# Kernel optimization log

Measured on AMD Instinct MI355X. Metric: run time of the kernel, lower is better.

The kernel has to match this reference:

```python
import jax, jax.numpy as jnp
import numpy as np

B, IN, OUT = 2048, 64, 2048


def setup_inputs() -> dict:
    key = jax.random.key(0)
    k1, k2, k3 = jax.random.split(key, 3)
    x = jax.random.normal(k1, (B, IN), dtype=jnp.float32)
    # learned params (shapes per init: means [in, out], inv_std_dev [out, in, in])
    means = jax.random.uniform(k2, (IN, OUT), dtype=jnp.float32)
    # roughly like the inverse of a diagonal step matrix plus small noise
    inv_std_dev = (jax.random.normal(k3, (OUT, IN, IN), dtype=jnp.float32) * 0.05
                   + jnp.eye(IN, dtype=jnp.float32) * 0.5)
    return {"x": x, "means": means, "inv_std_dev": inv_std_dev}


def reference(x, means, inv_std_dev):
    # diff[b, o, i] = x[b, i] - means[i, o]   -> [B, OUT, IN]
    d = x[:, None, :] - means.T[None, :, :]
    # torch uses inv_std_dev.pow(2) (elementwise square), not a matrix square
    A = inv_std_dev * inv_std_dev  # [OUT, IN, IN]
    # per-neuron quadratic form: q[b, o] = d[b,o,:] @ A[o] @ d[b,o,:]
    q = jnp.einsum('boi,oij,boj->bo', d, A, d)
    return jnp.exp(-0.5 * q)  # [B, OUT]
```

## Files before the change

### kernel.cpp

```cpp
#include <hip/hip_runtime.h>
#include <hip/hip_bf16.h>

typedef __bf16 bf16x8 __attribute__((ext_vector_type(8)));
typedef float f32x4 __attribute__((ext_vector_type(4)));
typedef float f32x16 __attribute__((ext_vector_type(16)));

#define B_N 2048
#define O_N 2048
#define K_N 64

__device__ __forceinline__ void gld16(const void* g, void* l) {
    __builtin_amdgcn_global_load_lds(
        (const __attribute__((address_space(1))) void*)g,
        (__attribute__((address_space(3))) void*)l,
        16, 0, 0);
}

__global__ __launch_bounds__(256) void rbf_prep(
    const float* __restrict__ inv, const float* __restrict__ means,
    __bf16* __restrict__ Atp, __bf16* __restrict__ cPhi,
    __bf16* __restrict__ cPlo, float* __restrict__ kArr)
{
    __shared__ float s[64 * 65];
    __shared__ float mld[64];
    __shared__ float uw[128];
    const int o = blockIdx.x;
    const int t = threadIdx.x;
    const float4* src = (const float4*)(inv + (size_t)o * 4096);
#pragma unroll
    for (int k = 0; k < 4; ++k) {
        const int idx = k * 256 + t;
        const float4 v = src[idx];
        const int i = idx >> 4;
        const int j0 = (idx & 15) * 4;
        s[i * 65 + j0 + 0] = v.x * v.x;
        s[i * 65 + j0 + 1] = v.y * v.y;
        s[i * 65 + j0 + 2] = v.z * v.z;
        s[i * 65 + j0 + 3] = v.w * v.w;
    }
    if (t < 64) mld[t] = means[(size_t)t * O_N + o];
    __syncthreads();
    if (t < 64) {
        float u = 0.f;
#pragma unroll
        for (int i = 0; i < 64; ++i) u = fmaf(s[i * 65 + t], mld[i], u);
        uw[t] = u;
    } else if (t < 128) {
        const int j = t - 64;
        float w = 0.f;
#pragma unroll
        for (int i = 0; i < 64; ++i) w = fmaf(s[j * 65 + i], mld[i], w);
        uw[64 + j] = w;
    }
    __syncthreads();
    if (t < 64) {
        const float c = -(uw[t] + uw[64 + t]);
        const __bf16 hi = (__bf16)c;
        const __bf16 lo = (__bf16)(c - (float)hi);
        const size_t eidx = (size_t)(o >> 5) * 2048 + (size_t)(t >> 4) * 512
                          + (size_t)(o & 31) * 16 + (t & 15);
        cPhi[eidx] = hi;
        cPlo[eidx] = lo;
    }
    if (t == 0) {
        float kk = 0.f;
#pragma unroll
        for (int j = 0; j < 64; ++j) kk = fmaf(uw[j], mld[j], kk);
        kArr[o] = kk;
    }
#pragma unroll
    for (int r = 0; r < 2; ++r) {
        const int ch = r * 256 + t;
        const int ss = ch >> 7;
        const int j = (ch >> 1) & 63;
        const int h = ch & 1;
        bf16x8 v;
#pragma unroll
        for (int e = 0; e < 8; ++e)
            v[e] = (__bf16)s[(16 * ss + 8 * h + e) * 65 + j];
        *(bf16x8*)(Atp + (size_t)o * 4096 + (size_t)ch * 8) = v;
    }
}

__global__ __launch_bounds__(256, 4) void rbf_main(
    const float* __restrict__ x, const __bf16* __restrict__ Atp,
    const __bf16* __restrict__ cPhi, const __bf16* __restrict__ cPlo,
    const float* __restrict__ kArr, float* __restrict__ out)
{
    __shared__ __align__(16) __bf16 sA[2][4096];
    __shared__ __align__(16) float sLin[4][32][32];
    __shared__ float sK[32];

    const int tid = threadIdx.x;
    const int wave = tid >> 6;
    const int lane = tid & 63;
    const int b = lane & 31;
    const int h = lane >> 5;

    const int wg = (int)blockIdx.x;
    const int xcd = wg & 7;
    const int loc = wg >> 3;
    const int og = xcd * 8 + (loc >> 4);
    const int bg = loc & 15;
    const int oBase = og * 32;
    const int rowW = bg * 128 + wave * 32;
    const int row = rowW + b;
    const float* xr = x + (size_t)row * K_N;

    const f32x16 zz = {0.f,0.f,0.f,0.f,0.f,0.f,0.f,0.f,
                       0.f,0.f,0.f,0.f,0.f,0.f,0.f,0.f};

    bf16x8 xh[4], xl[4];
#pragma unroll
    for (int ss = 0; ss < 4; ++ss) {
        const float* p = xr + ss * 16 + h * 8;
        bf16x8 vh, vl;
#pragma unroll
        for (int e = 0; e < 8; ++e) {
            const float v = p[e];
            const __bf16 hi = (__bf16)v;
            vh[e] = hi;
            vl[e] = (__bf16)(v - (float)hi);
        }
        xh[ss] = vh; xl[ss] = vl;
    }
    f32x4 xd[2][4];
#pragma unroll
    for (int mt = 0; mt < 2; ++mt)
#pragma unroll
        for (int rq = 0; rq < 4; ++rq)
            xd[mt][rq] = *(const f32x4*)(xr + mt * 32 + rq * 8 + h * 4);

    {
        const __bf16* ch = cPhi + (size_t)og * 2048;
        const __bf16* cl = cPlo + (size_t)og * 2048;
        f32x16 lin = zz;
#pragma unroll
        for (int ss = 0; ss < 4; ++ss) {
            const bf16x8 fh = *(const bf16x8*)(ch + ss * 512 + b * 16 + h * 8);
            const bf16x8 fl = *(const bf16x8*)(cl + ss * 512 + b * 16 + h * 8);
            lin = __builtin_amdgcn_mfma_f32_32x32x16_bf16(fh, xh[ss], lin, 0, 0, 0);
            lin = __builtin_amdgcn_mfma_f32_32x32x16_bf16(fh, xl[ss], lin, 0, 0, 0);
            lin = __builtin_amdgcn_mfma_f32_32x32x16_bf16(fl, xh[ss], lin, 0, 0, 0);
        }
#pragma unroll
        for (int r = 0; r < 16; ++r)
            sLin[wave][(r & 3) + 8 * (r >> 2) + 4 * h][b] = lin[r];
    }
    if (tid < 32) sK[tid] = kArr[oBase + tid];

    const int L0 = tid * 16;
    const int L1 = 4096 + tid * 16;
    const int S0 = L0 ^ (((L0 >> 7) & 7) << 4);
    const int S1 = L1 ^ (((L1 >> 7) & 7) << 4);
    const char* gp = (const char*)(Atp + (size_t)oBase * 4096);
    gld16(gp + S0, (char*)&sA[0][0] + L0);
    gld16(gp + S1, (char*)&sA[0][0] + L1);

    const int off0 = (b * 32 + h * 16) ^ (((b >> 2) & 7) << 4);

    float q4[4];
#pragma unroll 4
    for (int i = 0; i < 32; ++i) {
        __syncthreads();
        if (i < 31) {
            const char* gn = gp + (size_t)(i + 1) * 8192;
            char* ld = (char*)&sA[(i + 1) & 1][0];
            gld16(gn + S0, ld + L0);
            gld16(gn + S1, ld + L1);
        }
        const char* bufp = (const char*)&sA[i & 1][0];

        f32x16 acc0 = zz, acc1 = zz;
#pragma unroll
        for (int ss = 0; ss < 4; ++ss) {
            const bf16x8 a0 = *(const bf16x8*)(bufp + ss * 2048 + off0);
            acc0 = __builtin_amdgcn_mfma_f32_32x32x16_bf16(a0, xh[ss], acc0, 0, 0, 0);
        }
#pragma unroll
        for (int ss = 0; ss < 4; ++ss) {
            const bf16x8 a1 = *(const bf16x8*)(bufp + ss * 2048 + 1024 + off0);
            acc1 = __builtin_amdgcn_mfma_f32_32x32x16_bf16(a1, xh[ss], acc1, 0, 0, 0);
        }

        float p[4] = {0.f, 0.f, 0.f, 0.f};
#pragma unroll
        for (int rg = 0; rg < 4; ++rg)
#pragma unroll
            for (int e = 0; e < 4; ++e)
                p[rg] = fmaf(acc0[rg * 4 + e], xd[0][rg][e], p[rg]);
#pragma unroll
        for (int rg = 0; rg < 4; ++rg)
#pragma unroll
            for (int e = 0; e < 4; ++e)
                p[rg] = fmaf(acc1[rg * 4 + e], xd[1][rg][e], p[rg]);
        float q = (p[0] + p[1]) + (p[2] + p[3]);
        q += __shfl_xor(q, 32, 64);
        q += sLin[wave][i][b];
        const float ev = exp2f((q + sK[i]) * -0.72134752044448170368f);
        q4[i & 3] = ev;

        if ((i & 3) == 3 && h == 0) {
            const f32x4 v = {q4[0], q4[1], q4[2], q4[3]};
            *(f32x4*)(out + (size_t)row * O_N + oBase + (i - 3)) = v;
        }
    }
}

extern "C" void kernel_launch(void* const* d_in, const int* in_sizes, int n_in,
                              void* d_out, int out_size, void* d_ws, size_t ws_size,
                              hipStream_t stream)
{
    const float* x = (const float*)d_in[0];
    const float* means = (const float*)d_in[1];
    const float* inv = (const float*)d_in[2];
    float* out = (float*)d_out;

    char* w = (char*)d_ws;
    __bf16* Atp  = (__bf16*)w;
    __bf16* cPhi = (__bf16*)(w + (size_t)O_N * 4096 * 2);
    __bf16* cPlo = (__bf16*)(w + (size_t)O_N * 4096 * 2 + 262144);
    float*  kArr = (float*)(w + (size_t)O_N * 4096 * 2 + 524288);

    rbf_prep<<<dim3(O_N), dim3(256), 0, stream>>>(inv, means, Atp, cPhi, cPlo, kArr);
    rbf_main<<<dim3(1024), dim3(256), 0, stream>>>(x, Atp, cPhi, cPlo, kArr, out);

    (void)in_sizes; (void)n_in; (void)out_size; (void)ws_size;
}
```

Before: 64.54 us.

## Double rows per wave, triple-buffer A tiles with explicit waitcnt pipeline

Each wave now handles 64 batch rows instead of 32, so every A tile loaded into LDS is reused across twice as many MFMAs, and the grid is halved to 512 workgroups. The LDS ring grows from double to triple buffering with a two-ahead prefetch, manual barriers and vmcnt waits, and s_setprio around the MFMA block. Outputs are now written as scalar stores per element instead of packed float4 stores. Launch bounds drop to 2 waves per SIMD to fit the extra registers, which lowers occupancy and may under-fill the 256 CUs with only 512 blocks.

```diff
diff --git a/kernel.cpp b/kernel.cpp
--- a/kernel.cpp
+++ b/kernel.cpp
@@ -73,22 +73,22 @@
         const int ch = r * 256 + t;
         const int ss = ch >> 7;
         const int j = (ch >> 1) & 63;
-        const int h = ch & 1;
+        const int hh = ch & 1;
         bf16x8 v;
 #pragma unroll
         for (int e = 0; e < 8; ++e)
-            v[e] = (__bf16)s[(16 * ss + 8 * h + e) * 65 + j];
+            v[e] = (__bf16)s[(16 * ss + 8 * hh + e) * 65 + j];
         *(bf16x8*)(Atp + (size_t)o * 4096 + (size_t)ch * 8) = v;
     }
 }
 
-__global__ __launch_bounds__(256, 4) void rbf_main(
+__global__ __launch_bounds__(256, 2) void rbf_main(
     const float* __restrict__ x, const __bf16* __restrict__ Atp,
     const __bf16* __restrict__ cPhi, const __bf16* __restrict__ cPlo,
     const float* __restrict__ kArr, float* __restrict__ out)
 {
-    __shared__ __align__(16) __bf16 sA[2][4096];
-    __shared__ __align__(16) float sLin[4][32][32];
+    __shared__ __align__(16) __bf16 sA[3][4096];
+    __shared__ __align__(16) float sLin[4][32][64];
     __shared__ float sK[32];
 
     const int tid = threadIdx.x;
@@ -100,111 +100,159 @@
     const int wg = (int)blockIdx.x;
     const int xcd = wg & 7;
     const int loc = wg >> 3;
-    const int og = xcd * 8 + (loc >> 4);
-    const int bg = loc & 15;
+    const int og = xcd * 8 + (loc >> 3);
+    const int bg = loc & 7;
     const int oBase = og * 32;
-    const int rowW = bg * 128 + wave * 32;
-    const int row = rowW + b;
-    const float* xr = x + (size_t)row * K_N;
+    const int rowW = bg * 256 + wave * 64;
+
+    const float* xr0 = x + (size_t)(rowW + b) * K_N;
+    const float* xr1 = x + (size_t)(rowW + 32 + b) * K_N;
 
     const f32x16 zz = {0.f,0.f,0.f,0.f,0.f,0.f,0.f,0.f,
                        0.f,0.f,0.f,0.f,0.f,0.f,0.f,0.f};
 
-    bf16x8 xh[4], xl[4];
-#pragma unroll
-    for (int ss = 0; ss < 4; ++ss) {
-        const float* p = xr + ss * 16 + h * 8;
-        bf16x8 vh, vl;
-#pragma unroll
-        for (int e = 0; e < 8; ++e) {
-            const float v = p[e];
-            const __bf16 hi = (__bf16)v;
-            vh[e] = hi;
-            vl[e] = (__bf16)(v - (float)hi);
-        }
-        xh[ss] = vh; xl[ss] = vl;
-    }
-    f32x4 xd[2][4];
-#pragma unroll
-    for (int mt = 0; mt < 2; ++mt)
-#pragma unroll
-        for (int rq = 0; rq < 4; ++rq)
-            xd[mt][rq] = *(const f32x4*)(xr + mt * 32 + rq * 8 + h * 4);
-
+    bf16x8 xh[2][4];
+    f32x4 xd[2][2][4];
     {
-        const __bf16* ch = cPhi + (size_t)og * 2048;
-        const __bf16* cl = cPlo + (size_t)og * 2048;
-        f32x16 lin = zz;
+        bf16x8 xl[2][4];
+#pragma unroll
+        for (int t = 0; t < 2; ++t) {
+            const float* xr = t ? xr1 : xr0;
+#pragma unroll
+            for (int ss = 0; ss < 4; ++ss) {
+                const float* p = xr + ss * 16 + h * 8;
+                bf16x8 vh, vl;
+#pragma unroll
+                for (int e = 0; e < 8; ++e) {
+                    const float v = p[e];
+                    const __bf16 hi = (__bf16)v;
+                    vh[e] = hi;
+                    vl[e] = (__bf16)(v - (float)hi);
+                }
+                xh[t][ss] = vh; xl[t][ss] = vl;
+            }
+#pragma unroll
+            for (int mt = 0; mt < 2; ++mt)
+#pragma unroll
+                for (int rq = 0; rq < 4; ++rq)
+                    xd[t][mt][rq] = *(const f32x4*)(xr + mt * 32 + rq * 8 + h * 4);
+        }
+        const __bf16* chp = cPhi + (size_t)og * 2048;
+        const __bf16* clp = cPlo + (size_t)og * 2048;
+        bf16x8 fh[4], fl[4];
 #pragma unroll
         for (int ss = 0; ss < 4; ++ss) {
-            const bf16x8 fh = *(const bf16x8*)(ch + ss * 512 + b * 16 + h * 8);
-            const bf16x8 fl = *(const bf16x8*)(cl + ss * 512 + b * 16 + h * 8);
-            lin = __builtin_amdgcn_mfma_f32_32x32x16_bf16(fh, xh[ss], lin, 0, 0, 0);
-            lin = __builtin_amdgcn_mfma_f32_32x32x16_bf16(fh, xl[ss], lin, 0, 0, 0);
-            lin = __builtin_amdgcn_mfma_f32_32x32x16_bf16(fl, xh[ss], lin, 0, 0, 0);
-        }
-#pragma unroll
-        for (int r = 0; r < 16; ++r)
-            sLin[wave][(r & 3) + 8 * (r >> 2) + 4 * h][b] = lin[r];
+            fh[ss] = *(const bf16x8*)(chp + ss * 512 + b * 16 + h * 8);
+            fl[ss] = *(const bf16x8*)(clp + ss * 512 + b * 16 + h * 8);
+        }
+#pragma unroll
+        for (int t = 0; t < 2; ++t) {
+            f32x16 lin = zz;
+#pragma unroll
+            for (int ss = 0; ss < 4; ++ss) {
+                lin = __builtin_amdgcn_mfma_f32_32x32x16_bf16(fh[ss], xh[t][ss], lin, 0, 0, 0);
+                lin = __builtin_amdgcn_mfma_f32_32x32x16_bf16(fh[ss], xl[t][ss], lin, 0, 0, 0);
+                lin = __builtin_amdgcn_mfma_f32_32x32x16_bf16(fl[ss], xh[t][ss], lin, 0, 0, 0);
+            }
+#pragma unroll
+            for (int r = 0; r < 16; ++r)
+                sLin[wave][(r & 3) + 8 * (r >> 2) + 4 * h][t * 32 + b] = lin[r];
+        }
     }
     if (tid < 32) sK[tid] = kArr[oBase + tid];
-
-    const int L0 = tid * 16;
-    const int L1 = 4096 + tid * 16;
+    __syncthreads();
+
+    const int L0 = tid * 16, L1 = 4096 + tid * 16;
     const int S0 = L0 ^ (((L0 >> 7) & 7) << 4);
     const int S1 = L1 ^ (((L1 >> 7) & 7) << 4);
     const char* gp = (const char*)(Atp + (size_t)oBase * 4096);
     gld16(gp + S0, (char*)&sA[0][0] + L0);
     gld16(gp + S1, (char*)&sA[0][0] + L1);
+    gld16(gp + 8192 + S0, (char*)&sA[1][0] + L0);
+    gld16(gp + 8192 + S1, (char*)&sA[1][0] + L1);
 
     const int off0 = (b * 32 + h * 16) ^ (((b >> 2) & 7) << 4);
-
-    float q4[4];
-#pragma unroll 4
-    for (int i = 0; i < 32; ++i) {
-        __syncthreads();
-        if (i < 31) {
-            const char* gn = gp + (size_t)(i + 1) * 8192;
-            char* ld = (char*)&sA[(i + 1) & 1][0];
-            gld16(gn + S0, ld + L0);
-            gld16(gn + S1, ld + L1);
-        }
-        const char* bufp = (const char*)&sA[i & 1][0];
-
-        f32x16 acc0 = zz, acc1 = zz;
+    float* o0 = out + (size_t)(rowW + b) * O_N + oBase;
+    float* o1 = out + (size_t)(rowW + 32 + b) * O_N + oBase;
+
+    auto body = [&](int i, const __bf16* bufp) {
+        __builtin_amdgcn_s_setprio(1);
+        f32x16 a00 = zz, a01 = zz, a10 = zz, a11 = zz;
 #pragma unroll
         for (int ss = 0; ss < 4; ++ss) {
-            const bf16x8 a0 = *(const bf16x8*)(bufp + ss * 2048 + off0);
-            acc0 = __builtin_amdgcn_mfma_f32_32x32x16_bf16(a0, xh[ss], acc0, 0, 0, 0);
-        }
-#pragma unroll
-        for (int ss = 0; ss < 4; ++ss) {
-            const bf16x8 a1 = *(const bf16x8*)(bufp + ss * 2048 + 1024 + off0);
-            acc1 = __builtin_amdgcn_mfma_f32_32x32x16_bf16(a1, xh[ss], acc1, 0, 0, 0);
-        }
-
-        float p[4] = {0.f, 0.f, 0.f, 0.f};
-#pragma unroll
-        for (int rg = 0; rg < 4; ++rg)
-#pragma unroll
-            for (int e = 0; e < 4; ++e)
-                p[rg] = fmaf(acc0[rg * 4 + e], xd[0][rg][e], p[rg]);
-#pragma unroll
-        for (int rg = 0; rg < 4; ++rg)
-#pragma unroll
-            for (int e = 0; e < 4; ++e)
-                p[rg] = fmaf(acc1[rg * 4 + e], xd[1][rg][e], p[rg]);
-        float q = (p[0] + p[1]) + (p[2] + p[3]);
-        q += __shfl_xor(q, 32, 64);
-        q += sLin[wave][i][b];
-        const float ev = exp2f((q + sK[i]) * -0.72134752044448170368f);
-        q4[i & 3] = ev;
-
-        if ((i & 3) == 3 && h == 0) {
-            const f32x4 v = {q4[0], q4[1], q4[2], q4[3]};
-            *(f32x4*)(out + (size_t)row * O_N + oBase + (i - 3)) = v;
-        }
-    }
+            const char* base = (const char*)bufp + ss * 2048;
+            const bf16x8 f0 = *(const bf16x8*)(base + off0);
+            const bf16x8 f1 = *(const bf16x8*)(base + 1024 + off0);
+            a00 = __builtin_amdgcn_mfma_f32_32x32x16_bf16(f0, xh[0][ss], a00, 0, 0, 0);
+            a10 = __builtin_amdgcn_mfma_f32_32x32x16_bf16(f0, xh[1][ss], a10, 0, 0, 0);
+            a01 = __builtin_amdgcn_mfma_f32_32x32x16_bf16(f1, xh[0][ss], a01, 0, 0, 0);
+            a11 = __builtin_amdgcn_mfma_f32_32x32x16_bf16(f1, xh[1][ss], a11, 0, 0, 0);
+        }
+        __builtin_amdgcn_s_setprio(0);
+        const float kk = sK[i];
+        {
+            float p0 = 0.f, p1 = 0.f, p2 = 0.f, p3 = 0.f;
+#pragma unroll
+            for (int e = 0; e < 4; ++e) {
+                p0 = fmaf(a00[e],      xd[0][0][0][e], p0);
+                p1 = fmaf(a00[4 + e],  xd[0][0][1][e], p1);
+                p2 = fmaf(a00[8 + e],  xd[0][0][2][e], p2);
+                p3 = fmaf(a00[12 + e], xd[0][0][3][e], p3);
+                p0 = fmaf(a01[e],      xd[0][1][0][e], p0);
+                p1 = fmaf(a01[4 + e],  xd[0][1][1][e], p1);
+                p2 = fmaf(a01[8 + e],  xd[0][1][2][e], p2);
+                p3 = fmaf(a01[12 + e], xd[0][1][3][e], p3);
+            }
+            float q = (p0 + p1) + (p2 + p3);
+            q += __shfl_xor(q, 32, 64);
+            q += sLin[wave][i][b] + kk;
+            const float ev = exp2f(q * -0.72134752044448170368f);
+            if (h == 0) o0[i] = ev;
+        }
+        {
+            float p0 = 0.f, p1 = 0.f, p2 = 0.f, p3 = 0.f;
+#pragma unroll
+            for (int e = 0; e < 4; ++e) {
+                p0 = fmaf(a10[e],      xd[1][0][0][e], p0);
+                p1 = fmaf(a10[4 + e],  xd[1][0][1][e], p1);
+                p2 = fmaf(a10[8 + e],  xd[1][0][2][e], p2);
+                p3 = fmaf(a10[12 + e], xd[1][0][3][e], p3);
+                p0 = fmaf(a11[e],      xd[1][1][0][e], p0);
+                p1 = fmaf(a11[4 + e],  xd[1][1][1][e], p1);
+                p2 = fmaf(a11[8 + e],  xd[1][1][2][e], p2);
+                p3 = fmaf(a11[12 + e], xd[1][1][3][e], p3);
+            }
+            float q = (p0 + p1) + (p2 + p3);
+            q += __shfl_xor(q, 32, 64);
+            q += sLin[wave][i][32 + b] + kk;
+            const float ev = exp2f(q * -0.72134752044448170368f);
+            if (h == 0) o1[i] = ev;
+        }
+    };
+
+#define RBF_ITER(I, BR, BW, WAIT) do {                                   \
+    __builtin_amdgcn_s_barrier();          \
+    __builtin_amdgcn_sched_barrier(0);                                   \
+    { const int pf_ = ((I) + 2 <= 31) ? ((I) + 2) : 31;                  \
+      const char* gn_ = gp + (size_t)pf_ * 8192;                         \
+      gld16(gn_ + S0, (char*)&sA[(BW)][0] + L0);                         \
+      gld16(gn_ + S1, (char*)&sA[(BW)][0] + L1); }                       \
+    asm volatile("s_waitcnt " WAIT ::: "memory");                        \
+    __builtin_amdgcn_s_barrier();              \
+    __builtin_amdgcn_sched_barrier(0);                                   \
+    body((I), (const __bf16*)&sA[(BR)][0]);                              \
+} while (0)
+
+    RBF_ITER(0, 0, 2, "vmcnt(4)");
+    RBF_ITER(1, 1, 0, "vmcnt(6)");
+#pragma unroll 1
+    for (int ii = 0; ii < 10; ++ii) {
+        const int i = 2 + ii * 3;
+        RBF_ITER(i,     2, 1, "vmcnt(8)");
+        RBF_ITER(i + 1, 0, 2, "vmcnt(8)");
+        RBF_ITER(i + 2, 1, 0, "vmcnt(8)");
+    }
+#undef RBF_ITER
 }
 
 extern "C" void kernel_launch(void* const* d_in, const int* in_sizes, int n_in,
@@ -223,7 +271,7 @@
     float*  kArr = (float*)(w + (size_t)O_N * 4096 * 2 + 524288);
 
     rbf_prep<<<dim3(O_N), dim3(256), 0, stream>>>(inv, means, Atp, cPhi, cPlo, kArr);
-    rbf_main<<<dim3(1024), dim3(256), 0, stream>>>(x, Atp, cPhi, cPlo, kArr, out);
+    rbf_main<<<dim3(512), dim3(256), 0, stream>>>(x, Atp, cPhi, cPlo, kArr, out);
 
     (void)in_sizes; (void)n_in; (void)out_size; (void)ws_size;
 }
```

After: 64.07 us. No clear change (-0.7%).
